# Performance work log

Measured on AMD Instinct MI355X. Metric: run time of the kernel, lower is better.

The kernel has to match this reference:

```python
import jax, jax.numpy as jnp
import numpy as np

N, L, S = 512, 1024, 32   # batch, latent dim, spatial (S*S == L)
F = 32 * S * S            # flattened encoder conv features (last conv = 32 ch)
H = 512                   # hidden width of latent MLP heads


def _lrelu(x):
    return jnp.where(x >= 0, x, 0.01 * x)


def _bn(x):
    # BatchNorm2d in training mode, gamma=1, beta=0 (default init)
    m = x.mean((0, 2, 3), keepdims=True)
    v = x.var((0, 2, 3), keepdims=True)
    return (x - m) * jax.lax.rsqrt(v + 1e-5)


def _conv(x, w, b):
    y = jax.lax.conv_general_dilated(x, w, (1, 1), 'SAME',
                                     dimension_numbers=('NCHW', 'OIHW', 'NCHW'))
    return y + b[None, :, None, None]


def _block(x, w, b):
    return _lrelu(_bn(_conv(x, w, b)))


def setup_inputs() -> dict:
    key = jax.random.key(0)
    ks = jax.random.split(key, 16)
    r = lambda k, s, sc: jax.random.normal(k, s, jnp.float32) * sc
    return {
        'x': r(ks[0], (N, 1, S, S), 1.0),
        'eps_c': r(ks[1], (N, L), 1.0),
        'eps_s': r(ks[2], (N, L), 1.0),
        'enc_cw1': r(ks[3], (2, 32, 1, 3, 3), 0.1),   'enc_cb1': jnp.zeros((2, 32)),
        'enc_cw2': r(ks[4], (2, 64, 32, 3, 3), 0.05), 'enc_cb2': jnp.zeros((2, 64)),
        'enc_cw3': r(ks[5], (2, 32, 64, 3, 3), 0.05), 'enc_cb3': jnp.zeros((2, 32)),
        'enc_muW1': r(ks[6], (2, H, F), 0.005), 'enc_muB1': jnp.zeros((2, H)),
        'enc_muW2': r(ks[7], (2, L, H), 0.02),  'enc_muB2': jnp.zeros((2, L)),
        'enc_vaW1': r(ks[8], (2, H, F), 0.005), 'enc_vaB1': jnp.zeros((2, H)),
        'enc_vaW2': r(ks[9], (2, L, H), 0.02),  'enc_vaB2': jnp.zeros((2, L)),
        'dec_cw1': r(ks[10], (2, 32, 1, 3, 3), 0.1),   'dec_cb1': jnp.zeros((2, 32)),
        'dec_cw2': r(ks[11], (2, 64, 32, 3, 3), 0.05), 'dec_cb2': jnp.zeros((2, 64)),
        'dec_cw3': r(ks[12], (2, 1, 64, 3, 3), 0.05),  'dec_cb3': jnp.zeros((2, 1)),
    }


def reference(x, eps_c, eps_s,
              enc_cw1, enc_cb1, enc_cw2, enc_cb2, enc_cw3, enc_cb3,
              enc_muW1, enc_muB1, enc_muW2, enc_muB2,
              enc_vaW1, enc_vaB1, enc_vaW2, enc_vaB2,
              dec_cw1, dec_cb1, dec_cw2, dec_cb2, dec_cw3, dec_cb3):
    def encode(i):
        h = _block(x, enc_cw1[i], enc_cb1[i])
        h = _block(h, enc_cw2[i], enc_cb2[i])
        h = _block(h, enc_cw3[i], enc_cb3[i])
        f = h.reshape(N, -1)                                   # [N, F]
        mu = _lrelu(_lrelu(f @ enc_muW1[i].T + enc_muB1[i]) @ enc_muW2[i].T + enc_muB2[i])
        lv = _lrelu(_lrelu(f @ enc_vaW1[i].T + enc_vaB1[i]) @ enc_vaW2[i].T + enc_vaB2[i])
        return mu, lv                                          # each [N, L]

    def decode(z, i):
        h = z.reshape(N, 1, S, S)
        h = _block(h, dec_cw1[i], dec_cb1[i])
        h = _block(h, dec_cw2[i], dec_cb2[i])
        h = _block(h, dec_cw3[i], dec_cb3[i])
        return h.reshape(N, 1, S, S)

    class_mu, class_logvar = encode(0)
    style_mu, style_logvar = encode(1)

    # precision-weighted product-of-experts group evidence (vectorized)
    precision = jnp.exp(-style_logvar)                  # 1/var, [N, L]
    group_var = 1.0 / precision.sum(0)                  # [L]
    group_mu = (style_mu * precision).sum(0) * group_var  # [L]
    group_logvar = jnp.log(group_var)

    # reparameterize
    z_c = eps_c * jnp.exp(0.5 * class_logvar) + class_mu          # [N, L]
    z_s = eps_s * jnp.exp(0.5 * group_logvar)[None] + group_mu[None]  # [N, L]

    output_c = decode(z_c, 0)
    output_s = jax.nn.relu(decode(z_s, 1))
    output = output_c * output_s                        # [N, 1, S, S]

    kl1 = -0.5 * jnp.sum(1.0 + class_logvar) + 0.5 * (
        jnp.sum(class_mu ** 2) + jnp.sum(jnp.exp(class_logvar) ** 2))
    kl2 = -0.5 * jnp.sum(1.0 + group_logvar) + 0.5 * (
        jnp.sum(group_mu ** 2) + jnp.sum(jnp.exp(group_logvar) ** 2))
    recon = (jnp.exp(x) - jnp.exp(output)) ** 2
    loss = -kl1 + kl2 + recon                           # [N, 1, S, S]
    return loss, output
```

## Files before the change

### kernel.cpp

```cpp
#include <hip/hip_runtime.h>

constexpr int N_   = 512;
constexpr int PIX  = 1024;
constexpr int L_   = 1024;
constexpr int F_   = 32768;
constexpr int H_   = 512;
constexpr float IC_ = 1.0f / (float)(512 * 1024);

__device__ __forceinline__ float lrelu(float t) { return t >= 0.f ? t : 0.01f * t; }

using frag  = __attribute__((ext_vector_type(8))) short;
using f32x4 = __attribute__((ext_vector_type(4))) float;
using s4    = __attribute__((ext_vector_type(4))) short;

#define BAR() do {                                              \
    asm volatile("s_waitcnt lgkmcnt(0)" ::: "memory");          \
    __builtin_amdgcn_s_barrier();                               \
    asm volatile("" ::: "memory");                              \
} while (0)

__device__ __forceinline__ void split_bf16(float v, short& hi, short& lo) {
    const unsigned b = __float_as_uint(v);
    hi = (short)(b >> 16);
    const float hf = __uint_as_float(b & 0xFFFF0000u);
    lo = (short)(__float_as_uint(v - hf) >> 16);
}

__device__ __forceinline__ frag ld2(const short* p) {
    union { frag f; struct { unsigned long long a, b; } u; } x;
    x.u.a = *(const unsigned long long*)(p);
    x.u.b = *(const unsigned long long*)(p + 4);
    return x.f;
}

__global__ __launch_bounds__(256) void wsplit6_kernel(
    const float* __restrict__ w0, const float* __restrict__ w1,
    const float* __restrict__ w2, const float* __restrict__ w3,
    const float* __restrict__ w4, const float* __restrict__ w5,
    short* __restrict__ hi, short* __restrict__ lo)
{
    const int layer = blockIdx.y;
    const float* W = layer == 0 ? w0 : layer == 1 ? w1 : layer == 2 ? w2 :
                     layer == 3 ? w3 : layer == 4 ? w4 : w5;
    const int CIN  = (layer == 1 || layer == 3) ? 64 : 32;
    const int NCOT = (layer == 1 || layer == 3) ? 2 : 4;
    const int idx = blockIdx.x * 256 + threadIdx.x;
    const int j    = idx & 7;
    const int lane = (idx >> 3) & 63;
    const int q    = lane >> 4, lm = lane & 15;
    const int blk  = idx >> 9;
    const int cot  = blk % NCOT;
    const int rest = blk / NCOT;
    const int pos  = rest % 9;
    const int cc   = rest / 9;
    const int co = cot * 16 + lm;
    const int ci = cc * 32 + q * 8 + j;
    short h, l;
    split_bf16(W[((size_t)co * CIN + ci) * 9 + pos], h, l);
    hi[layer * 18432 + idx] = h;
    lo[layer * 18432 + idx] = l;
}

template<int CIN, int COUT, bool BN_IN>
__global__ __launch_bounds__(256) void conv_mfma(
    const float* __restrict__ in, const short* __restrict__ wh,
    const short* __restrict__ wl, const float* __restrict__ bias,
    float* __restrict__ out, const float* __restrict__ stats_in,
    float* __restrict__ stats_out)
{
    constexpr int NCOT = COUT / 16;
    constexpr int NCH  = CIN / 32;
    constexpr int STR  = 36;
    constexpr int PLsh = 340 * STR;
    __shared__ __align__(16) short hiL[PLsh];
    __shared__ __align__(16) short loL[PLsh];
    __shared__ float red[2 * COUT];
    __shared__ float bnm[64], bni[64];
    const int tid  = threadIdx.x;
    const int n    = blockIdx.x >> 2;
    const int y0   = (blockIdx.x & 3) << 3;
    const int lane = tid & 63;
    const int wv   = tid >> 6;
    const int lm   = lane & 15;
    const int q    = lane >> 4;

    if (tid < 2 * COUT) red[tid] = 0.f;
    if (BN_IN && tid < CIN) {
        const float m  = stats_in[tid] * IC_;
        const float qq = stats_in[CIN + tid] * IC_;
        bnm[tid] = m;
        bni[tid] = rsqrtf(qq - m * m + 1e-5f);
    }
    __syncthreads();

    f32x4 acc[NCOT][4];
#pragma unroll
    for (int t = 0; t < NCOT; ++t)
#pragma unroll
        for (int pt = 0; pt < 4; ++pt) acc[t][pt] = {0.f, 0.f, 0.f, 0.f};

    const int rs0 = tid / 34, cs0 = tid % 34;
    const int idx1 = tid + 256;
    const int rs1 = idx1 / 34, cs1 = idx1 % 34;
    const int gr0 = y0 - 1 + rs0, gc0 = cs0 - 1;
    const int gr1 = y0 - 1 + rs1, gc1 = cs1 - 1;
    const bool in1 = idx1 < 340;
    const bool ok0 = ((unsigned)gr0 < 32u) && ((unsigned)gc0 < 32u);
    const bool ok1 = in1 && ((unsigned)gr1 < 32u) && ((unsigned)gc1 < 32u);
    const int  po0 = gr0 * 32 + gc0;
    const int  po1 = gr1 * 32 + gc1;

    const float* inb = in + ((size_t)n * CIN << 10);

    frag ahA[NCOT], alA[NCOT], ahB[NCOT], alB[NCOT];

    auto LDW = [&](frag (&dh)[NCOT], frag (&dl)[NCOT], int posAbs) {
#pragma unroll
        for (int t = 0; t < NCOT; ++t) {
            const size_t wb = (size_t)((posAbs * NCOT + t) * 512 + lane * 8);
            dh[t] = *(const frag*)&wh[wb];
            dl[t] = *(const frag*)&wl[wb];
        }
    };

    auto COMPUTE = [&](int pos, frag (&fh)[NCOT], frag (&fl)[NCOT]) {
        const int ky = pos / 3, kx = pos - ky * 3;
        __builtin_amdgcn_s_setprio(1);
#pragma unroll
        for (int pt = 0; pt < 4; ++pt) {
            const int ptile = wv * 4 + pt;
            const int row = ptile >> 1;
            const int col = ((ptile & 1) << 4) + lm;
            const int loff = ((row + ky) * 34 + col + kx) * STR + q * 8;
            const frag bh = ld2(&hiL[loff]);
            const frag bl = ld2(&loL[loff]);
#pragma unroll
            for (int t = 0; t < NCOT; ++t) {
                acc[t][pt] = __builtin_amdgcn_mfma_f32_16x16x32_bf16(
                    fh[t], bh, acc[t][pt], 0, 0, 0);
                acc[t][pt] = __builtin_amdgcn_mfma_f32_16x16x32_bf16(
                    fh[t], bl, acc[t][pt], 0, 0, 0);
                acc[t][pt] = __builtin_amdgcn_mfma_f32_16x16x32_bf16(
                    fl[t], bh, acc[t][pt], 0, 0, 0);
            }
        }
        __builtin_amdgcn_s_setprio(0);
    };

#pragma unroll 1
    for (int cc = 0; cc < NCH; ++cc) {
        if (cc) BAR();

        LDW(ahA, alA, cc * 9 + 0);

        {
            float v0r[32], v1r[32];
#pragma unroll
            for (int u = 0; u < 32; ++u) {
                const int cg = cc * 32 + u;
                v0r[u] = ok0 ? inb[((size_t)cg << 10) + po0] : 0.f;
                v1r[u] = ok1 ? inb[((size_t)cg << 10) + po1] : 0.f;
            }
#pragma unroll
            for (int u4 = 0; u4 < 32; u4 += 4) {
                s4 h0v, l0v, h1v, l1v;
#pragma unroll
                for (int e = 0; e < 4; ++e) {
                    const int ci = u4 + e;
                    const int cg = cc * 32 + ci;
                    float v0 = v0r[ci];
                    if (BN_IN && ok0) v0 = lrelu((v0 - bnm[cg]) * bni[cg]);
                    short h, l;
                    split_bf16(v0, h, l);
                    h0v[e] = h; l0v[e] = l;
                    float v1 = v1r[ci];
                    if (BN_IN && ok1) v1 = lrelu((v1 - bnm[cg]) * bni[cg]);
                    short h1, l1;
                    split_bf16(v1, h1, l1);
                    h1v[e] = h1; l1v[e] = l1;
                }
                *(s4*)&hiL[tid * STR + u4] = h0v;
                *(s4*)&loL[tid * STR + u4] = l0v;
                if (in1) {
                    *(s4*)&hiL[idx1 * STR + u4] = h1v;
                    *(s4*)&loL[idx1 * STR + u4] = l1v;
                }
            }
        }
        BAR();

#pragma unroll 1
        for (int pos = 0; pos < 8; pos += 2) {
            LDW(ahB, alB, cc * 9 + pos + 1);
            COMPUTE(pos, ahA, alA);
            LDW(ahA, alA, cc * 9 + pos + 2);
            COMPUTE(pos + 1, ahB, alB);
        }
        COMPUTE(8, ahA, alA);
    }

    float* ob = out + ((size_t)n * COUT << 10);
#pragma unroll
    for (int t = 0; t < NCOT; ++t) {
#pragma unroll
        for (int r = 0; r < 4; ++r) {
            const int co = t * 16 + q * 4 + r;
            const float b = bias[co];
            float s = 0.f, sq = 0.f;
#pragma unroll
            for (int pt = 0; pt < 4; ++pt) {
                const float v = acc[t][pt][r] + b;
                ob[((size_t)co << 10) + (y0 << 5) + ((wv * 4 + pt) << 4) + lm] = v;
                s += v; sq += v * v;
            }
#pragma unroll
            for (int off = 8; off > 0; off >>= 1) {
                s  += __shfl_down(s, off, 64);
                sq += __shfl_down(sq, off, 64);
            }
            if (lm == 0) {
                atomicAdd(&red[co], s);
                atomicAdd(&red[COUT + co], sq);
            }
        }
    }
    __syncthreads();
    if (tid < 2 * COUT) atomicAdd(&stats_out[tid], red[tid]);
}

template<int CIN, int COPB, bool BN_IN>
__global__ __launch_bounds__(256) void conv3x3(
    const float* __restrict__ in, const float* __restrict__ w,
    const float* __restrict__ bias, float* __restrict__ out,
    const float* __restrict__ stats_in, float* __restrict__ stats_out,
    int Cout)
{
    constexpr int CT = (CIN < 4) ? CIN : 4;
    __shared__ float tile[CT * PIX];
    __shared__ float red[2 * COPB];
    const int groups = Cout / COPB;
    const int n   = blockIdx.x / groups;
    const int co0 = (blockIdx.x % groups) * COPB;
    const int tid = threadIdx.x;
    const int x   = tid & 31;
    const int y0  = (tid >> 5) * 4;

    float acc[COPB][4];
#pragma unroll
    for (int c = 0; c < COPB; ++c)
#pragma unroll
        for (int j = 0; j < 4; ++j) acc[c][j] = 0.f;

    const float* inbase = in + (size_t)n * CIN * PIX;

#pragma unroll 1
    for (int s0 = 0; s0 < CIN; s0 += CT) {
        __syncthreads();
#pragma unroll
        for (int s = 0; s < CT; ++s) {
            float4 v = ((const float4*)(inbase + (size_t)(s0 + s) * PIX))[tid];
            if (BN_IN) {
                const int c = s0 + s;
                const float m   = stats_in[c] * IC_;
                const float q   = stats_in[CIN + c] * IC_;
                const float inv = rsqrtf(q - m * m + 1e-5f);
                v.x = lrelu((v.x - m) * inv);
                v.y = lrelu((v.y - m) * inv);
                v.z = lrelu((v.z - m) * inv);
                v.w = lrelu((v.w - m) * inv);
            }
            ((float4*)tile)[s * 256 + tid] = v;
        }
        __syncthreads();
#pragma unroll 2
        for (int s = 0; s < CT; ++s) {
            const int ci = s0 + s;
            const float* tp = tile + s * PIX;
            float r[6][3];
#pragma unroll
            for (int ry = 0; ry < 6; ++ry) {
                const int yy = y0 + ry - 1;
                const bool yok = (unsigned)yy < 32u;
#pragma unroll
                for (int cx = 0; cx < 3; ++cx) {
                    const int xx = x + cx - 1;
                    const bool ok = yok && ((unsigned)xx < 32u);
                    r[ry][cx] = ok ? tp[yy * 32 + xx] : 0.f;
                }
            }
#pragma unroll
            for (int c = 0; c < COPB; ++c) {
                const float* wp = w + ((size_t)(co0 + c) * CIN + ci) * 9;
#pragma unroll
                for (int ky = 0; ky < 3; ++ky)
#pragma unroll
                    for (int kx = 0; kx < 3; ++kx) {
                        const float wv = wp[ky * 3 + kx];
#pragma unroll
                        for (int j = 0; j < 4; ++j)
                            acc[c][j] += r[ky + j][kx] * wv;
                    }
            }
        }
    }

    if (tid < 2 * COPB) red[tid] = 0.f;
    __syncthreads();
#pragma unroll
    for (int c = 0; c < COPB; ++c) {
        const float b = bias[co0 + c];
        float* ob = out + (((size_t)n * Cout + co0 + c) << 10);
        float s = 0.f, q = 0.f;
#pragma unroll
        for (int j = 0; j < 4; ++j) {
            const float v = acc[c][j] + b;
            ob[(y0 + j) * 32 + x] = v;
            s += v; q += v * v;
        }
#pragma unroll
        for (int off = 32; off > 0; off >>= 1) {
            s += __shfl_down(s, off, 64);
            q += __shfl_down(q, off, 64);
        }
        if ((tid & 63) == 0) {
            atomicAdd(&red[c], s);
            atomicAdd(&red[COPB + c], q);
        }
    }
    __syncthreads();
    if (tid < COPB)
        atomicAdd(&stats_out[co0 + tid], red[tid]);
    else if (tid < 2 * COPB)
        atomicAdd(&stats_out[Cout + co0 + tid - COPB], red[tid]);
}

template<bool BN_A>
__global__ __launch_bounds__(256) void gemm_mfma(
    const float* __restrict__ A0, const float* __restrict__ A1,
    const float* __restrict__ B0, const float* __restrict__ B1,
    float* __restrict__ C0, float* __restrict__ C1,
    int K, int Nh, int kchunk, int xph,
    const float* __restrict__ bnstats, int Cin)
{
    __shared__ short AhL[4096], AlL[4096], BhL[4096], BlL[4096];
    const int tid  = threadIdx.x;
    const int head = blockIdx.x / xph;
    const int n0   = (blockIdx.x % xph) * 128;
    const int m0   = blockIdx.y * 128;
    const float* A = head ? A1 : A0;
    const float* B = head ? B1 : B0;
    float*       C = head ? C1 : C0;
    const int k0 = blockIdx.z * kchunk;
    const int k1 = k0 + kchunk;

    const int lane = tid & 63;
    const int wv   = tid >> 6;
    const int wm   = wv & 1;
    const int wn   = wv >> 1;
    const int lm   = lane & 15;
    const int q    = lane >> 4;

    const int srow = tid >> 1;
    const int smt  = srow >> 4;
    const int slm  = srow & 15;
    const int sq0  = (tid & 1) * 2;
    const int ks   = (tid & 1) * 16;

    float bnm0 = 0.f, bni0 = 1.f, bnm1 = 0.f, bni1 = 1.f;
    if (BN_A) {
        const int c0 = k0 >> 10;
        bnm0 = bnstats[c0] * IC_;
        const float q0 = bnstats[Cin + c0] * IC_;
        bni0 = rsqrtf(q0 - bnm0 * bnm0 + 1e-5f);
        const int c1 = (c0 + 1 < Cin) ? c0 + 1 : c0;
        bnm1 = bnstats[c1] * IC_;
        const float q1 = bnstats[Cin + c1] * IC_;
        bni1 = rsqrtf(q1 - bnm1 * bnm1 + 1e-5f);
    }

    f32x4 acc[4][4];
#pragma unroll
    for (int i = 0; i < 4; ++i)
#pragma unroll
        for (int j = 0; j < 4; ++j) acc[i][j] = {0.f, 0.f, 0.f, 0.f};

    auto cv8 = [](float4 u, float4 w2, frag& h, frag& l) {
        const float v[8] = {u.x, u.y, u.z, u.w, w2.x, w2.y, w2.z, w2.w};
#pragma unroll
        for (int e = 0; e < 8; ++e) {
            short hh, ll;
            split_bf16(v[e], hh, ll);
            h[e] = hh; l[e] = ll;
        }
    };

    float4 aA[4], bA[4], aB[4], bB[4];

    auto LOADAB = [&](float4 (&a4)[4], float4 (&b4)[4], int kb) {
        const float* Ap = A + (size_t)(m0 + srow) * K + kb + ks;
        const float* Bp = B + (size_t)(n0 + srow) * K + kb + ks;
#pragma unroll
        for (int g = 0; g < 4; ++g) a4[g] = ((const float4*)Ap)[g];
#pragma unroll
        for (int g = 0; g < 4; ++g) b4[g] = ((const float4*)Bp)[g];
    };

    auto STEP = [&](float4 (&a4)[4], float4 (&b4)[4], int kb, int kpf) {
        if (BN_A) {
            const int sel = (kb - k0) >> 10;
            const float m   = sel ? bnm1 : bnm0;
            const float inv = sel ? bni1 : bni0;
#pragma unroll
            for (int g = 0; g < 4; ++g) {
                a4[g].x = lrelu((a4[g].x - m) * inv);
                a4[g].y = lrelu((a4[g].y - m) * inv);
                a4[g].z = lrelu((a4[g].z - m) * inv);
                a4[g].w = lrelu((a4[g].w - m) * inv);
            }
        }

        frag ah0, al0, ah1, al1, bh0, bl0, bh1, bl1;
        cv8(a4[0], a4[1], ah0, al0);
        cv8(a4[2], a4[3], ah1, al1);
        cv8(b4[0], b4[1], bh0, bl0);
        cv8(b4[2], b4[3], bh1, bl1);

        if (kpf < k1) LOADAB(a4, b4, kpf);

        BAR();
        const int o0 = ((smt * 4 + sq0) * 16 + slm) * 8;
        const int o1 = ((smt * 4 + sq0 + 1) * 16 + slm) * 8;
        *(frag*)&AhL[o0] = ah0;  *(frag*)&AhL[o1] = ah1;
        *(frag*)&AlL[o0] = al0;  *(frag*)&AlL[o1] = al1;
        *(frag*)&BhL[o0] = bh0;  *(frag*)&BhL[o1] = bh1;
        *(frag*)&BlL[o0] = bl0;  *(frag*)&BlL[o1] = bl1;
        BAR();

        frag fah[4], fal[4], fbh[4], fbl[4];
#pragma unroll
        for (int t = 0; t < 4; ++t) {
            const int oa = (((wm * 4 + t) * 4 + q) * 16 + lm) * 8;
            const int ob = (((wn * 4 + t) * 4 + q) * 16 + lm) * 8;
            fah[t] = *(const frag*)&AhL[oa];
            fal[t] = *(const frag*)&AlL[oa];
            fbh[t] = *(const frag*)&BhL[ob];
            fbl[t] = *(const frag*)&BlL[ob];
        }

#pragma unroll
        for (int i = 0; i < 4; ++i)
#pragma unroll
            for (int j = 0; j < 4; ++j) {
                acc[i][j] = __builtin_amdgcn_mfma_f32_16x16x32_bf16(
                    fah[i], fbh[j], acc[i][j], 0, 0, 0);
                acc[i][j] = __builtin_amdgcn_mfma_f32_16x16x32_bf16(
                    fah[i], fbl[j], acc[i][j], 0, 0, 0);
                acc[i][j] = __builtin_amdgcn_mfma_f32_16x16x32_bf16(
                    fal[i], fbh[j], acc[i][j], 0, 0, 0);
            }
    };

    LOADAB(aA, bA, k0);
    LOADAB(aB, bB, k0 + 32);

#pragma unroll 1
    for (int kb = k0; kb < k1; kb += 64) {
        STEP(aA, bA, kb,      kb + 64);
        STEP(aB, bB, kb + 32, kb + 96);
    }

#pragma unroll
    for (int i = 0; i < 4; ++i) {
        const int m = m0 + wm * 64 + i * 16 + q * 4;
#pragma unroll
        for (int j = 0; j < 4; ++j) {
            const int n = n0 + wn * 64 + j * 16 + lm;
            float* cp = C + (size_t)m * Nh + n;
#pragma unroll
            for (int r = 0; r < 4; ++r)
                atomicAdd(cp + (size_t)r * Nh, acc[i][j][r]);
        }
    }
}

__global__ __launch_bounds__(256) void bias_lrelu2_kernel(
    float* __restrict__ bufa, const float* __restrict__ ba,
    float* __restrict__ bufb, const float* __restrict__ bb,
    int Nn, int per)
{
    const int idx = blockIdx.x * 256 + threadIdx.x;
    if (idx < per) {
        bufa[idx] = lrelu(bufa[idx] + ba[idx % Nn]);
    } else {
        const int j = idx - per;
        bufb[j] = lrelu(bufb[j] + bb[j % Nn]);
    }
}

__device__ __forceinline__ void block_reduce_atomic(float t, float* target)
{
#pragma unroll
    for (int off = 32; off > 0; off >>= 1) t += __shfl_down(t, off, 64);
    __shared__ float lt[4];
    const int wave = threadIdx.x >> 6, lane = threadIdx.x & 63;
    if (lane == 0) lt[wave] = t;
    __syncthreads();
    if (threadIdx.x == 0) atomicAdd(target, lt[0] + lt[1] + lt[2] + lt[3]);
}

__global__ __launch_bounds__(256) void poe_kernel(
    const float* __restrict__ mu1, const float* __restrict__ lv1,
    float* __restrict__ gmu, float* __restrict__ glv, float* __restrict__ kl)
{
    const int l = blockIdx.x * 256 + threadIdx.x;
    float sp = 0.f, sm = 0.f;
    for (int n = 0; n < N_; ++n) {
        const float lv = lv1[(size_t)n * L_ + l];
        const float p  = expf(-lv);
        sp += p;
        sm += mu1[(size_t)n * L_ + l] * p;
    }
    const float gv = 1.f / sp;
    const float gm = sm * gv;
    const float gl = -logf(sp);
    gmu[l] = gm;
    glv[l] = gl;
    const float t = -0.5f * (1.f + gl) + 0.5f * (gm * gm + gv * gv);
    block_reduce_atomic(t, &kl[1]);
}

__global__ __launch_bounds__(256) void reparam_kernel(
    const float* __restrict__ mu0, const float* __restrict__ lv0,
    const float* __restrict__ eps_c, const float* __restrict__ eps_s,
    const float* __restrict__ gmu, const float* __restrict__ glv,
    float* __restrict__ zc, float* __restrict__ zs, float* __restrict__ kl)
{
    const int idx = blockIdx.x * 256 + threadIdx.x;
    const int l = idx & (L_ - 1);
    const float m  = mu0[idx];
    const float lv = lv0[idx];
    zc[idx] = eps_c[idx] * expf(0.5f * lv) + m;
    zs[idx] = eps_s[idx] * expf(0.5f * glv[l]) + gmu[l];
    const float e = expf(lv);
    const float t = -0.5f * (1.f + lv) + 0.5f * (m * m + e * e);
    block_reduce_atomic(t, &kl[0]);
}

__global__ __launch_bounds__(256) void final_kernel(
    const float* __restrict__ x, const float* __restrict__ oc,
    const float* __restrict__ os, const float* __restrict__ stC,
    const float* __restrict__ stS, const float* __restrict__ kl,
    float* __restrict__ out)
{
    const int idx = blockIdx.x * 256 + threadIdx.x;
    const float mc = stC[0] * IC_, qc = stC[1] * IC_;
    const float ivc = rsqrtf(qc - mc * mc + 1e-5f);
    const float ms = stS[0] * IC_, qs = stS[1] * IC_;
    const float ivs = rsqrtf(qs - ms * ms + 1e-5f);
    const float tc = lrelu((oc[idx] - mc) * ivc);
    const float ts = fmaxf((os[idx] - ms) * ivs, 0.f);
    const float o = tc * ts;
    const float d = expf(x[idx]) - expf(o);
    out[idx]            = -kl[0] + kl[1] + d * d;
    out[N_ * PIX + idx] = o;
}

extern "C" void kernel_launch(void* const* d_in, const int* in_sizes, int n_in,
                              void* d_out, int out_size, void* d_ws, size_t ws_size,
                              hipStream_t stream)
{
    const float* x        = (const float*)d_in[0];
    const float* eps_c    = (const float*)d_in[1];
    const float* eps_s    = (const float*)d_in[2];
    const float* enc_cw1  = (const float*)d_in[3];
    const float* enc_cb1  = (const float*)d_in[4];
    const float* enc_cw2  = (const float*)d_in[5];
    const float* enc_cb2  = (const float*)d_in[6];
    const float* enc_cw3  = (const float*)d_in[7];
    const float* enc_cb3  = (const float*)d_in[8];
    const float* enc_muW1 = (const float*)d_in[9];
    const float* enc_muB1 = (const float*)d_in[10];
    const float* enc_muW2 = (const float*)d_in[11];
    const float* enc_muB2 = (const float*)d_in[12];
    const float* enc_vaW1 = (const float*)d_in[13];
    const float* enc_vaB1 = (const float*)d_in[14];
    const float* enc_vaW2 = (const float*)d_in[15];
    const float* enc_vaB2 = (const float*)d_in[16];
    const float* dec_cw1  = (const float*)d_in[17];
    const float* dec_cb1  = (const float*)d_in[18];
    const float* dec_cw2  = (const float*)d_in[19];
    const float* dec_cb2  = (const float*)d_in[20];
    const float* dec_cw3  = (const float*)d_in[21];
    const float* dec_cb3  = (const float*)d_in[22];
    float* out = (float*)d_out;

    float* ws   = (float*)d_ws;
    float* bufA = ws;
    float* bufB = bufA + (size_t)N_ * 64 * PIX;
    float* h1   = bufB + (size_t)N_ * 32 * PIX;
    float* h2   = h1 + N_ * H_;
    float* mu0  = h2 + N_ * H_;
    float* lv0  = mu0 + N_ * L_;
    float* mu1  = lv0 + N_ * L_;
    float* lv1  = mu1 + N_ * L_;
    float* zc   = lv1 + N_ * L_;
    float* zs   = zc + N_ * L_;
    float* oc   = zs + N_ * L_;
    float* os   = oc + N_ * L_;
    float* gmu  = os + N_ * L_;
    float* glv  = gmu + L_;
    float* stats = glv + L_;
    float* kl   = stats + 12 * 128;
    short* wsh  = (short*)(kl + 4);
    short* wsl  = wsh + 6 * 18432;

    auto st  = [&](int s) { return stats + 128 * s; };
    auto whp = [&](int layer) { return wsh + layer * 18432; };
    auto wlp = [&](int layer) { return wsl + layer * 18432; };

    hipMemsetAsync(stats, 0, (12 * 128 + 4) * sizeof(float), stream);

    wsplit6_kernel<<<dim3(72, 6), 256, 0, stream>>>(
        enc_cw2, enc_cw3, enc_cw2 + 64 * 32 * 9, enc_cw3 + 32 * 64 * 9,
        dec_cw2, dec_cw2 + 64 * 32 * 9, wsh, wsl);

    for (int i = 0; i < 2; ++i) {
        const float* cw1 = enc_cw1 + (size_t)i * 32 * 9;
        const float* cb1 = enc_cb1 + (size_t)i * 32;
        const float* cb2 = enc_cb2 + (size_t)i * 64;
        const float* cb3 = enc_cb3 + (size_t)i * 32;

        conv3x3<1, 16, false><<<N_ * 2, 256, 0, stream>>>(
            x, cw1, cb1, bufB, nullptr, st(i * 3 + 0), 32);
        conv_mfma<32, 64, true><<<N_ * 4, 256, 0, stream>>>(
            bufB, whp(i * 2), wlp(i * 2), cb2, bufA, st(i * 3 + 0), st(i * 3 + 1));
        conv_mfma<64, 32, true><<<N_ * 4, 256, 0, stream>>>(
            bufA, whp(i * 2 + 1), wlp(i * 2 + 1), cb3, bufB, st(i * 3 + 1), st(i * 3 + 2));

        const float* W1m = enc_muW1 + (size_t)i * H_ * F_;
        const float* B1m = enc_muB1 + (size_t)i * H_;
        const float* W2m = enc_muW2 + (size_t)i * L_ * H_;
        const float* B2m = enc_muB2 + (size_t)i * L_;
        const float* W1v = enc_vaW1 + (size_t)i * H_ * F_;
        const float* B1v = enc_vaB1 + (size_t)i * H_;
        const float* W2v = enc_vaW2 + (size_t)i * L_ * H_;
        const float* B2v = enc_vaB2 + (size_t)i * L_;
        float* mu_i = (i == 0) ? mu0 : mu1;
        float* lv_i = (i == 0) ? lv0 : lv1;

        hipMemsetAsync(h1, 0, (size_t)2 * N_ * H_ * sizeof(float), stream);
        gemm_mfma<true><<<dim3(8, 4, 16), 256, 0, stream>>>(
            bufB, bufB, W1m, W1v, h1, h2, F_, H_, 2048, 4, st(i * 3 + 2), 32);
        bias_lrelu2_kernel<<<(2 * N_ * H_) / 256, 256, 0, stream>>>(
            h1, B1m, h2, B1v, H_, N_ * H_);

        hipMemsetAsync(mu_i, 0, (size_t)2 * N_ * L_ * sizeof(float), stream);
        gemm_mfma<false><<<dim3(16, 4, 4), 256, 0, stream>>>(
            h1, h2, W2m, W2v, mu_i, lv_i, H_, L_, 128, 8, nullptr, 0);
        bias_lrelu2_kernel<<<(2 * N_ * L_) / 256, 256, 0, stream>>>(
            mu_i, B2m, lv_i, B2v, L_, N_ * L_);
    }

    poe_kernel<<<L_ / 256, 256, 0, stream>>>(mu1, lv1, gmu, glv, kl);
    reparam_kernel<<<(N_ * L_) / 256, 256, 0, stream>>>(
        mu0, lv0, eps_c, eps_s, gmu, glv, zc, zs, kl);

    for (int i = 0; i < 2; ++i) {
        const float* cw1 = dec_cw1 + (size_t)i * 32 * 9;
        const float* cb1 = dec_cb1 + (size_t)i * 32;
        const float* cb2 = dec_cb2 + (size_t)i * 64;
        const float* cw3 = dec_cw3 + (size_t)i * 64 * 9;
        const float* cb3 = dec_cb3 + (size_t)i * 1;
        const float* zi = (i == 0) ? zc : zs;
        float* oi = (i == 0) ? oc : os;

        conv3x3<1, 16, false><<<N_ * 2, 256, 0, stream>>>(
            zi, cw1, cb1, bufB, nullptr, st(6 + i * 3 + 0), 32);
        conv_mfma<32, 64, true><<<N_ * 4, 256, 0, stream>>>(
            bufB, whp(4 + i), wlp(4 + i), cb2, bufA, st(6 + i * 3 + 0), st(6 + i * 3 + 1));
        conv3x3<64, 1, true><<<N_, 256, 0, stream>>>(
            bufA, cw3, cb3, oi, st(6 + i * 3 + 1), st(6 + i * 3 + 2), 1);
    }

    final_kernel<<<(N_ * PIX) / 256, 256, 0, stream>>>(
        x, oc, os, st(8), st(11), kl, out);
}
```

Measured before the change: 1.460 ms.

## Shrink conv tiles to 4 rows and double-buffer GEMM shared memory staging

The MFMA conv kernel now handles 4 output rows per block instead of 8, doubling the grid. It stages the input halo in 8-channel batches to cut register pressure, and requests 4 blocks per CU through launch bounds. The split-bf16 GEMM gets double-buffered LDS with one barrier per k-step, letting MMA on one stage overlap staging of the next, and raises MFMA priority. The second-layer GEMM's k-split doubles to give more blocks. The costs are more halo reloads per conv block, twice the GEMM LDS footprint, and more atomic adds in the split-K GEMM.

```diff
diff --git a/kernel.cpp b/kernel.cpp
--- a/kernel.cpp
+++ b/kernel.cpp
@@ -62,7 +62,7 @@
 }
 
 template<int CIN, int COUT, bool BN_IN>
-__global__ __launch_bounds__(256) void conv_mfma(
+__global__ __launch_bounds__(256, 4) void conv_mfma(
     const float* __restrict__ in, const short* __restrict__ wh,
     const short* __restrict__ wl, const float* __restrict__ bias,
     float* __restrict__ out, const float* __restrict__ stats_in,
@@ -71,14 +71,14 @@
     constexpr int NCOT = COUT / 16;
     constexpr int NCH  = CIN / 32;
     constexpr int STR  = 36;
-    constexpr int PLsh = 340 * STR;
+    constexpr int PLsh = 204 * STR;
     __shared__ __align__(16) short hiL[PLsh];
     __shared__ __align__(16) short loL[PLsh];
     __shared__ float red[2 * COUT];
     __shared__ float bnm[64], bni[64];
     const int tid  = threadIdx.x;
-    const int n    = blockIdx.x >> 2;
-    const int y0   = (blockIdx.x & 3) << 3;
+    const int n    = blockIdx.x >> 3;
+    const int y0   = (blockIdx.x & 7) << 2;
     const int lane = tid & 63;
     const int wv   = tid >> 6;
     const int lm   = lane & 15;
@@ -93,22 +93,17 @@
     }
     __syncthreads();
 
-    f32x4 acc[NCOT][4];
+    f32x4 acc[NCOT][2];
 #pragma unroll
     for (int t = 0; t < NCOT; ++t)
 #pragma unroll
-        for (int pt = 0; pt < 4; ++pt) acc[t][pt] = {0.f, 0.f, 0.f, 0.f};
+        for (int pt = 0; pt < 2; ++pt) acc[t][pt] = {0.f, 0.f, 0.f, 0.f};
 
     const int rs0 = tid / 34, cs0 = tid % 34;
-    const int idx1 = tid + 256;
-    const int rs1 = idx1 / 34, cs1 = idx1 % 34;
     const int gr0 = y0 - 1 + rs0, gc0 = cs0 - 1;
-    const int gr1 = y0 - 1 + rs1, gc1 = cs1 - 1;
-    const bool in1 = idx1 < 340;
-    const bool ok0 = ((unsigned)gr0 < 32u) && ((unsigned)gc0 < 32u);
-    const bool ok1 = in1 && ((unsigned)gr1 < 32u) && ((unsigned)gc1 < 32u);
+    const bool act = tid < 204;
+    const bool ok0 = act && ((unsigned)gr0 < 32u) && ((unsigned)gc0 < 32u);
     const int  po0 = gr0 * 32 + gc0;
-    const int  po1 = gr1 * 32 + gc1;
 
     const float* inb = in + ((size_t)n * CIN << 10);
 
@@ -127,8 +122,8 @@
         const int ky = pos / 3, kx = pos - ky * 3;
         __builtin_amdgcn_s_setprio(1);
 #pragma unroll
-        for (int pt = 0; pt < 4; ++pt) {
-            const int ptile = wv * 4 + pt;
+        for (int pt = 0; pt < 2; ++pt) {
+            const int ptile = wv * 2 + pt;
             const int row = ptile >> 1;
             const int col = ((ptile & 1) << 4) + lm;
             const int loff = ((row + ky) * 34 + col + kx) * STR + q * 8;
@@ -153,37 +148,30 @@
 
         LDW(ahA, alA, cc * 9 + 0);
 
-        {
-            float v0r[32], v1r[32];
-#pragma unroll
-            for (int u = 0; u < 32; ++u) {
-                const int cg = cc * 32 + u;
+#pragma unroll 1
+        for (int cb = 0; cb < 32; cb += 8) {
+            float v0r[8];
+#pragma unroll
+            for (int u = 0; u < 8; ++u) {
+                const int cg = cc * 32 + cb + u;
                 v0r[u] = ok0 ? inb[((size_t)cg << 10) + po0] : 0.f;
-                v1r[u] = ok1 ? inb[((size_t)cg << 10) + po1] : 0.f;
-            }
-#pragma unroll
-            for (int u4 = 0; u4 < 32; u4 += 4) {
-                s4 h0v, l0v, h1v, l1v;
-#pragma unroll
-                for (int e = 0; e < 4; ++e) {
-                    const int ci = u4 + e;
-                    const int cg = cc * 32 + ci;
-                    float v0 = v0r[ci];
-                    if (BN_IN && ok0) v0 = lrelu((v0 - bnm[cg]) * bni[cg]);
-                    short h, l;
-                    split_bf16(v0, h, l);
-                    h0v[e] = h; l0v[e] = l;
-                    float v1 = v1r[ci];
-                    if (BN_IN && ok1) v1 = lrelu((v1 - bnm[cg]) * bni[cg]);
-                    short h1, l1;
-                    split_bf16(v1, h1, l1);
-                    h1v[e] = h1; l1v[e] = l1;
-                }
-                *(s4*)&hiL[tid * STR + u4] = h0v;
-                *(s4*)&loL[tid * STR + u4] = l0v;
-                if (in1) {
-                    *(s4*)&hiL[idx1 * STR + u4] = h1v;
-                    *(s4*)&loL[idx1 * STR + u4] = l1v;
+            }
+            if (act) {
+#pragma unroll
+                for (int u4 = 0; u4 < 8; u4 += 4) {
+                    s4 h0v, l0v;
+#pragma unroll
+                    for (int e = 0; e < 4; ++e) {
+                        const int ci = cb + u4 + e;
+                        const int cg = cc * 32 + ci;
+                        float v0 = v0r[u4 + e];
+                        if (BN_IN && ok0) v0 = lrelu((v0 - bnm[cg]) * bni[cg]);
+                        short h, l;
+                        split_bf16(v0, h, l);
+                        h0v[e] = h; l0v[e] = l;
+                    }
+                    *(s4*)&hiL[tid * STR + cb + u4] = h0v;
+                    *(s4*)&loL[tid * STR + cb + u4] = l0v;
                 }
             }
         }
@@ -208,9 +196,10 @@
             const float b = bias[co];
             float s = 0.f, sq = 0.f;
 #pragma unroll
-            for (int pt = 0; pt < 4; ++pt) {
+            for (int pt = 0; pt < 2; ++pt) {
+                const int ptile = wv * 2 + pt;
                 const float v = acc[t][pt][r] + b;
-                ob[((size_t)co << 10) + (y0 << 5) + ((wv * 4 + pt) << 4) + lm] = v;
+                ob[((size_t)co << 10) + (y0 << 5) + (ptile << 4) + lm] = v;
                 s += v; sq += v * v;
             }
 #pragma unroll
@@ -342,7 +331,7 @@
     int K, int Nh, int kchunk, int xph,
     const float* __restrict__ bnstats, int Cin)
 {
-    __shared__ short AhL[4096], AlL[4096], BhL[4096], BlL[4096];
+    __shared__ short AhL[8192], AlL[8192], BhL[8192], BlL[8192];
     const int tid  = threadIdx.x;
     const int head = blockIdx.x / xph;
     const int n0   = (blockIdx.x % xph) * 128;
@@ -351,7 +340,6 @@
     const float* B = head ? B1 : B0;
     float*       C = head ? C1 : C0;
     const int k0 = blockIdx.z * kchunk;
-    const int k1 = k0 + kchunk;
 
     const int lane = tid & 63;
     const int wv   = tid >> 6;
@@ -394,9 +382,8 @@
         }
     };
 
-    float4 aA[4], bA[4], aB[4], bB[4];
-
-    auto LOADAB = [&](float4 (&a4)[4], float4 (&b4)[4], int kb) {
+    float4 a4[4], b4[4];
+    auto LOADAB = [&](int kb) {
         const float* Ap = A + (size_t)(m0 + srow) * K + kb + ks;
         const float* Bp = B + (size_t)(n0 + srow) * K + kb + ks;
 #pragma unroll
@@ -405,9 +392,12 @@
         for (int g = 0; g < 4; ++g) b4[g] = ((const float4*)Bp)[g];
     };
 
-    auto STEP = [&](float4 (&a4)[4], float4 (&b4)[4], int kb, int kpf) {
+    const int o0 = ((smt * 4 + sq0) * 16 + slm) * 8;
+    const int o1 = ((smt * 4 + sq0 + 1) * 16 + slm) * 8;
+
+    auto STAGE = [&](int s) {
         if (BN_A) {
-            const int sel = (kb - k0) >> 10;
+            const int sel = s >> 5;
             const float m   = sel ? bnm1 : bnm0;
             const float inv = sel ? bni1 : bni0;
 #pragma unroll
@@ -418,35 +408,31 @@
                 a4[g].w = lrelu((a4[g].w - m) * inv);
             }
         }
-
         frag ah0, al0, ah1, al1, bh0, bl0, bh1, bl1;
         cv8(a4[0], a4[1], ah0, al0);
         cv8(a4[2], a4[3], ah1, al1);
         cv8(b4[0], b4[1], bh0, bl0);
         cv8(b4[2], b4[3], bh1, bl1);
-
-        if (kpf < k1) LOADAB(a4, b4, kpf);
-
-        BAR();
-        const int o0 = ((smt * 4 + sq0) * 16 + slm) * 8;
-        const int o1 = ((smt * 4 + sq0 + 1) * 16 + slm) * 8;
-        *(frag*)&AhL[o0] = ah0;  *(frag*)&AhL[o1] = ah1;
-        *(frag*)&AlL[o0] = al0;  *(frag*)&AlL[o1] = al1;
-        *(frag*)&BhL[o0] = bh0;  *(frag*)&BhL[o1] = bh1;
-        *(frag*)&BlL[o0] = bl0;  *(frag*)&BlL[o1] = bl1;
-        BAR();
-
+        const int pb = (s & 1) << 12;
+        *(frag*)&AhL[pb + o0] = ah0;  *(frag*)&AhL[pb + o1] = ah1;
+        *(frag*)&AlL[pb + o0] = al0;  *(frag*)&AlL[pb + o1] = al1;
+        *(frag*)&BhL[pb + o0] = bh0;  *(frag*)&BhL[pb + o1] = bh1;
+        *(frag*)&BlL[pb + o0] = bl0;  *(frag*)&BlL[pb + o1] = bl1;
+    };
+
+    auto MMA = [&](int s) {
+        const int pb = (s & 1) << 12;
         frag fah[4], fal[4], fbh[4], fbl[4];
 #pragma unroll
         for (int t = 0; t < 4; ++t) {
-            const int oa = (((wm * 4 + t) * 4 + q) * 16 + lm) * 8;
-            const int ob = (((wn * 4 + t) * 4 + q) * 16 + lm) * 8;
+            const int oa = pb + (((wm * 4 + t) * 4 + q) * 16 + lm) * 8;
+            const int ob = pb + (((wn * 4 + t) * 4 + q) * 16 + lm) * 8;
             fah[t] = *(const frag*)&AhL[oa];
             fal[t] = *(const frag*)&AlL[oa];
             fbh[t] = *(const frag*)&BhL[ob];
             fbl[t] = *(const frag*)&BlL[ob];
         }
-
+        __builtin_amdgcn_s_setprio(1);
 #pragma unroll
         for (int i = 0; i < 4; ++i)
 #pragma unroll
@@ -458,16 +444,24 @@
                 acc[i][j] = __builtin_amdgcn_mfma_f32_16x16x32_bf16(
                     fal[i], fbh[j], acc[i][j], 0, 0, 0);
             }
+        __builtin_amdgcn_s_setprio(0);
     };
 
-    LOADAB(aA, bA, k0);
-    LOADAB(aB, bB, k0 + 32);
+    const int T = kchunk >> 5;
+
+    LOADAB(k0);
+    STAGE(0);
+    LOADAB(k0 + 32);
+    BAR();
 
 #pragma unroll 1
-    for (int kb = k0; kb < k1; kb += 64) {
-        STEP(aA, bA, kb,      kb + 64);
-        STEP(aB, bB, kb + 32, kb + 96);
-    }
+    for (int s = 1; s < T; ++s) {
+        MMA(s - 1);
+        STAGE(s);
+        if (s + 1 < T) LOADAB(k0 + (s + 1) * 32);
+        BAR();
+    }
+    MMA(T - 1);
 
 #pragma unroll
     for (int i = 0; i < 4; ++i) {
@@ -632,9 +626,9 @@
 
         conv3x3<1, 16, false><<<N_ * 2, 256, 0, stream>>>(
             x, cw1, cb1, bufB, nullptr, st(i * 3 + 0), 32);
-        conv_mfma<32, 64, true><<<N_ * 4, 256, 0, stream>>>(
+        conv_mfma<32, 64, true><<<N_ * 8, 256, 0, stream>>>(
             bufB, whp(i * 2), wlp(i * 2), cb2, bufA, st(i * 3 + 0), st(i * 3 + 1));
-        conv_mfma<64, 32, true><<<N_ * 4, 256, 0, stream>>>(
+        conv_mfma<64, 32, true><<<N_ * 8, 256, 0, stream>>>(
             bufA, whp(i * 2 + 1), wlp(i * 2 + 1), cb3, bufB, st(i * 3 + 1), st(i * 3 + 2));
 
         const float* W1m = enc_muW1 + (size_t)i * H_ * F_;
@@ -655,8 +649,8 @@
             h1, B1m, h2, B1v, H_, N_ * H_);
 
         hipMemsetAsync(mu_i, 0, (size_t)2 * N_ * L_ * sizeof(float), stream);
-        gemm_mfma<false><<<dim3(16, 4, 4), 256, 0, stream>>>(
-            h1, h2, W2m, W2v, mu_i, lv_i, H_, L_, 128, 8, nullptr, 0);
+        gemm_mfma<false><<<dim3(16, 4, 8), 256, 0, stream>>>(
+            h1, h2, W2m, W2v, mu_i, lv_i, H_, L_, 64, 8, nullptr, 0);
         bias_lrelu2_kernel<<<(2 * N_ * L_) / 256, 256, 0, stream>>>(
             mu_i, B2m, lv_i, B2v, L_, N_ * L_);
     }
@@ -676,7 +670,7 @@
 
         conv3x3<1, 16, false><<<N_ * 2, 256, 0, stream>>>(
             zi, cw1, cb1, bufB, nullptr, st(6 + i * 3 + 0), 32);
-        conv_mfma<32, 64, true><<<N_ * 4, 256, 0, stream>>>(
+        conv_mfma<32, 64, true><<<N_ * 8, 256, 0, stream>>>(
             bufB, whp(4 + i), wlp(4 + i), cb2, bufA, st(6 + i * 3 + 0), st(6 + i * 3 + 1));
         conv3x3<64, 1, true><<<N_, 256, 0, stream>>>(
             bufA, cw3, cb3, oi, st(6 + i * 3 + 1), st(6 + i * 3 + 2), 1);
```

Measured after the change: 1.626 ms. 1.11x slower.

## Fuse bias+LeakyReLU into GEMM consumers and double-buffer GEMM LDS staging

Applied to the files above, without the earlier changes.

Removes the bias_lrelu2 kernels. The first-layer bias and activation are applied while the second GEMM loads its A operand, and the second-layer bias and activation are applied inside the PoE and reparam kernels. The GEMM main loop is restructured to use double-buffered LDS with one barrier per k-step, and MFMA issue is raised in priority via s_setprio. This saves two elementwise passes per encoder and halves GEMM barriers, at the cost of doubled LDS usage, which may lower occupancy.

```diff
diff --git a/kernel.cpp b/kernel.cpp
--- a/kernel.cpp
+++ b/kernel.cpp
@@ -334,15 +334,16 @@
         atomicAdd(&stats_out[Cout + co0 + tid - COPB], red[tid]);
 }
 
-template<bool BN_A>
+template<int MODE>
 __global__ __launch_bounds__(256) void gemm_mfma(
     const float* __restrict__ A0, const float* __restrict__ A1,
     const float* __restrict__ B0, const float* __restrict__ B1,
     float* __restrict__ C0, float* __restrict__ C1,
     int K, int Nh, int kchunk, int xph,
-    const float* __restrict__ bnstats, int Cin)
-{
-    __shared__ short AhL[4096], AlL[4096], BhL[4096], BlL[4096];
+    const float* __restrict__ bnstats, int Cin,
+    const float* __restrict__ ba0, const float* __restrict__ ba1)
+{
+    __shared__ short AhL[8192], AlL[8192], BhL[8192], BlL[8192];
     const int tid  = threadIdx.x;
     const int head = blockIdx.x / xph;
     const int n0   = (blockIdx.x % xph) * 128;
@@ -350,8 +351,8 @@
     const float* A = head ? A1 : A0;
     const float* B = head ? B1 : B0;
     float*       C = head ? C1 : C0;
+    const float* BA = head ? ba1 : ba0;
     const int k0 = blockIdx.z * kchunk;
-    const int k1 = k0 + kchunk;
 
     const int lane = tid & 63;
     const int wv   = tid >> 6;
@@ -367,7 +368,7 @@
     const int ks   = (tid & 1) * 16;
 
     float bnm0 = 0.f, bni0 = 1.f, bnm1 = 0.f, bni1 = 1.f;
-    if (BN_A) {
+    if (MODE == 1) {
         const int c0 = k0 >> 10;
         bnm0 = bnstats[c0] * IC_;
         const float q0 = bnstats[Cin + c0] * IC_;
@@ -394,9 +395,8 @@
         }
     };
 
-    float4 aA[4], bA[4], aB[4], bB[4];
-
-    auto LOADAB = [&](float4 (&a4)[4], float4 (&b4)[4], int kb) {
+    float4 a4[4], b4[4];
+    auto LOADAB = [&](int kb) {
         const float* Ap = A + (size_t)(m0 + srow) * K + kb + ks;
         const float* Bp = B + (size_t)(n0 + srow) * K + kb + ks;
 #pragma unroll
@@ -405,9 +405,12 @@
         for (int g = 0; g < 4; ++g) b4[g] = ((const float4*)Bp)[g];
     };
 
-    auto STEP = [&](float4 (&a4)[4], float4 (&b4)[4], int kb, int kpf) {
-        if (BN_A) {
-            const int sel = (kb - k0) >> 10;
+    const int o0 = ((smt * 4 + sq0) * 16 + slm) * 8;
+    const int o1 = ((smt * 4 + sq0 + 1) * 16 + slm) * 8;
+
+    auto STAGE = [&](int s) {
+        if (MODE == 1) {
+            const int sel = s >> 5;
             const float m   = sel ? bnm1 : bnm0;
             const float inv = sel ? bni1 : bni0;
 #pragma unroll
@@ -418,35 +421,42 @@
                 a4[g].w = lrelu((a4[g].w - m) * inv);
             }
         }
-
+        if (MODE == 2) {
+            const float* bp = BA + k0 + s * 32 + ks;
+#pragma unroll
+            for (int g = 0; g < 4; ++g) {
+                const float4 bv = ((const float4*)bp)[g];
+                a4[g].x = lrelu(a4[g].x + bv.x);
+                a4[g].y = lrelu(a4[g].y + bv.y);
+                a4[g].z = lrelu(a4[g].z + bv.z);
+                a4[g].w = lrelu(a4[g].w + bv.w);
+            }
+        }
         frag ah0, al0, ah1, al1, bh0, bl0, bh1, bl1;
         cv8(a4[0], a4[1], ah0, al0);
         cv8(a4[2], a4[3], ah1, al1);
         cv8(b4[0], b4[1], bh0, bl0);
         cv8(b4[2], b4[3], bh1, bl1);
-
-        if (kpf < k1) LOADAB(a4, b4, kpf);
-
-        BAR();
-        const int o0 = ((smt * 4 + sq0) * 16 + slm) * 8;
-        const int o1 = ((smt * 4 + sq0 + 1) * 16 + slm) * 8;
-        *(frag*)&AhL[o0] = ah0;  *(frag*)&AhL[o1] = ah1;
-        *(frag*)&AlL[o0] = al0;  *(frag*)&AlL[o1] = al1;
-        *(frag*)&BhL[o0] = bh0;  *(frag*)&BhL[o1] = bh1;
-        *(frag*)&BlL[o0] = bl0;  *(frag*)&BlL[o1] = bl1;
-        BAR();
-
+        const int pb = (s & 1) << 12;
+        *(frag*)&AhL[pb + o0] = ah0;  *(frag*)&AhL[pb + o1] = ah1;
+        *(frag*)&AlL[pb + o0] = al0;  *(frag*)&AlL[pb + o1] = al1;
+        *(frag*)&BhL[pb + o0] = bh0;  *(frag*)&BhL[pb + o1] = bh1;
+        *(frag*)&BlL[pb + o0] = bl0;  *(frag*)&BlL[pb + o1] = bl1;
+    };
+
+    auto MMA = [&](int s) {
+        const int pb = (s & 1) << 12;
         frag fah[4], fal[4], fbh[4], fbl[4];
 #pragma unroll
         for (int t = 0; t < 4; ++t) {
-            const int oa = (((wm * 4 + t) * 4 + q) * 16 + lm) * 8;
-            const int ob = (((wn * 4 + t) * 4 + q) * 16 + lm) * 8;
+            const int oa = pb + (((wm * 4 + t) * 4 + q) * 16 + lm) * 8;
+            const int ob = pb + (((wn * 4 + t) * 4 + q) * 16 + lm) * 8;
             fah[t] = *(const frag*)&AhL[oa];
             fal[t] = *(const frag*)&AlL[oa];
             fbh[t] = *(const frag*)&BhL[ob];
             fbl[t] = *(const frag*)&BlL[ob];
         }
-
+        __builtin_amdgcn_s_setprio(1);
 #pragma unroll
         for (int i = 0; i < 4; ++i)
 #pragma unroll
@@ -458,16 +468,24 @@
                 acc[i][j] = __builtin_amdgcn_mfma_f32_16x16x32_bf16(
                     fal[i], fbh[j], acc[i][j], 0, 0, 0);
             }
+        __builtin_amdgcn_s_setprio(0);
     };
 
-    LOADAB(aA, bA, k0);
-    LOADAB(aB, bB, k0 + 32);
+    const int T = kchunk >> 5;
+
+    LOADAB(k0);
+    STAGE(0);
+    LOADAB(k0 + 32);
+    BAR();
 
 #pragma unroll 1
-    for (int kb = k0; kb < k1; kb += 64) {
-        STEP(aA, bA, kb,      kb + 64);
-        STEP(aB, bB, kb + 32, kb + 96);
-    }
+    for (int s = 1; s < T; ++s) {
+        MMA(s - 1);
+        STAGE(s);
+        if (s + 1 < T) LOADAB(k0 + (s + 1) * 32);
+        BAR();
+    }
+    MMA(T - 1);
 
 #pragma unroll
     for (int i = 0; i < 4; ++i) {
@@ -480,20 +498,6 @@
             for (int r = 0; r < 4; ++r)
                 atomicAdd(cp + (size_t)r * Nh, acc[i][j][r]);
         }
-    }
-}
-
-__global__ __launch_bounds__(256) void bias_lrelu2_kernel(
-    float* __restrict__ bufa, const float* __restrict__ ba,
-    float* __restrict__ bufb, const float* __restrict__ bb,
-    int Nn, int per)
-{
-    const int idx = blockIdx.x * 256 + threadIdx.x;
-    if (idx < per) {
-        bufa[idx] = lrelu(bufa[idx] + ba[idx % Nn]);
-    } else {
-        const int j = idx - per;
-        bufb[j] = lrelu(bufb[j] + bb[j % Nn]);
     }
 }
 
@@ -510,15 +514,17 @@
 
 __global__ __launch_bounds__(256) void poe_kernel(
     const float* __restrict__ mu1, const float* __restrict__ lv1,
+    const float* __restrict__ bmu, const float* __restrict__ blv,
     float* __restrict__ gmu, float* __restrict__ glv, float* __restrict__ kl)
 {
     const int l = blockIdx.x * 256 + threadIdx.x;
+    const float bm = bmu[l], bl = blv[l];
     float sp = 0.f, sm = 0.f;
     for (int n = 0; n < N_; ++n) {
-        const float lv = lv1[(size_t)n * L_ + l];
+        const float lv = lrelu(lv1[(size_t)n * L_ + l] + bl);
         const float p  = expf(-lv);
         sp += p;
-        sm += mu1[(size_t)n * L_ + l] * p;
+        sm += lrelu(mu1[(size_t)n * L_ + l] + bm) * p;
     }
     const float gv = 1.f / sp;
     const float gm = sm * gv;
@@ -531,14 +537,15 @@
 
 __global__ __launch_bounds__(256) void reparam_kernel(
     const float* __restrict__ mu0, const float* __restrict__ lv0,
+    const float* __restrict__ bmu, const float* __restrict__ blv,
     const float* __restrict__ eps_c, const float* __restrict__ eps_s,
     const float* __restrict__ gmu, const float* __restrict__ glv,
     float* __restrict__ zc, float* __restrict__ zs, float* __restrict__ kl)
 {
     const int idx = blockIdx.x * 256 + threadIdx.x;
     const int l = idx & (L_ - 1);
-    const float m  = mu0[idx];
-    const float lv = lv0[idx];
+    const float m  = lrelu(mu0[idx] + bmu[l]);
+    const float lv = lrelu(lv0[idx] + blv[l]);
     zc[idx] = eps_c[idx] * expf(0.5f * lv) + m;
     zs[idx] = eps_s[idx] * expf(0.5f * glv[l]) + gmu[l];
     const float e = expf(lv);
@@ -640,30 +647,27 @@
         const float* W1m = enc_muW1 + (size_t)i * H_ * F_;
         const float* B1m = enc_muB1 + (size_t)i * H_;
         const float* W2m = enc_muW2 + (size_t)i * L_ * H_;
-        const float* B2m = enc_muB2 + (size_t)i * L_;
         const float* W1v = enc_vaW1 + (size_t)i * H_ * F_;
         const float* B1v = enc_vaB1 + (size_t)i * H_;
         const float* W2v = enc_vaW2 + (size_t)i * L_ * H_;
-        const float* B2v = enc_vaB2 + (size_t)i * L_;
         float* mu_i = (i == 0) ? mu0 : mu1;
         float* lv_i = (i == 0) ? lv0 : lv1;
 
         hipMemsetAsync(h1, 0, (size_t)2 * N_ * H_ * sizeof(float), stream);
-        gemm_mfma<true><<<dim3(8, 4, 16), 256, 0, stream>>>(
-            bufB, bufB, W1m, W1v, h1, h2, F_, H_, 2048, 4, st(i * 3 + 2), 32);
-        bias_lrelu2_kernel<<<(2 * N_ * H_) / 256, 256, 0, stream>>>(
-            h1, B1m, h2, B1v, H_, N_ * H_);
+        gemm_mfma<1><<<dim3(8, 4, 16), 256, 0, stream>>>(
+            bufB, bufB, W1m, W1v, h1, h2, F_, H_, 2048, 4,
+            st(i * 3 + 2), 32, nullptr, nullptr);
 
         hipMemsetAsync(mu_i, 0, (size_t)2 * N_ * L_ * sizeof(float), stream);
-        gemm_mfma<false><<<dim3(16, 4, 4), 256, 0, stream>>>(
-            h1, h2, W2m, W2v, mu_i, lv_i, H_, L_, 128, 8, nullptr, 0);
-        bias_lrelu2_kernel<<<(2 * N_ * L_) / 256, 256, 0, stream>>>(
-            mu_i, B2m, lv_i, B2v, L_, N_ * L_);
-    }
-
-    poe_kernel<<<L_ / 256, 256, 0, stream>>>(mu1, lv1, gmu, glv, kl);
+        gemm_mfma<2><<<dim3(16, 4, 4), 256, 0, stream>>>(
+            h1, h2, W2m, W2v, mu_i, lv_i, H_, L_, 128, 8,
+            nullptr, 0, B1m, B1v);
+    }
+
+    poe_kernel<<<L_ / 256, 256, 0, stream>>>(
+        mu1, lv1, enc_muB2 + L_, enc_vaB2 + L_, gmu, glv, kl);
     reparam_kernel<<<(N_ * L_) / 256, 256, 0, stream>>>(
-        mu0, lv0, eps_c, eps_s, gmu, glv, zc, zs, kl);
+        mu0, lv0, enc_muB2, enc_vaB2, eps_c, eps_s, gmu, glv, zc, zs, kl);
 
     for (int i = 0; i < 2; ++i) {
         const float* cw1 = dec_cw1 + (size_t)i * 32 * 9;
```

Result: no change. 1.458 ms (-0.1%).
